# Kernel optimization log

Hardware: AMD Instinct MI355X
Metric: run time of the kernel (lower is better)

Reference implementation:

```python
import jax, jax.numpy as jnp
import numpy as np

DIM = 768
HEADS = 12
HEAD_DIM = DIM // HEADS
HIDDEN = 4 * DIM
SCALE = HEAD_DIM ** -0.5
LN_EPS = 1e-5


def _fit_poly_gelu():
    # replicate PolyGELU.__init__: quadratic least-squares fit to exact GELU on [-3,3]
    x = np.linspace(-3.0, 3.0, 10000).astype(np.float32)
    y = np.asarray(jax.nn.gelu(jnp.asarray(x), approximate=False))
    X = np.stack([x ** 2, x, np.ones_like(x)], axis=1)
    c, *_ = np.linalg.lstsq(X, y, rcond=None)
    return c.astype(np.float32)  # [a, b, c]


def setup_inputs() -> dict:
    key = jax.random.key(0)
    ks = jax.random.split(key, 8)
    g = _fit_poly_gelu()
    w = lambda k, shp: (jax.random.normal(k, shp, dtype=jnp.float32) * 0.02)
    return {
        "x": jax.random.normal(ks[0], (4, 2048, DIM), dtype=jnp.float32),
        "ln1_g": jnp.ones((DIM,), jnp.float32),
        "ln1_b": jnp.zeros((DIM,), jnp.float32),
        "ln2_g": jnp.ones((DIM,), jnp.float32),
        "ln2_b": jnp.zeros((DIM,), jnp.float32),
        "qkv_w": w(ks[1], (DIM, 3 * DIM)),   # stored [in, out]
        "qkv_b": jnp.zeros((3 * DIM,), jnp.float32),
        "proj_w": w(ks[2], (DIM, DIM)),
        "proj_b": jnp.zeros((DIM,), jnp.float32),
        "fc1_w": w(ks[3], (DIM, HIDDEN)),
        "fc1_b": jnp.zeros((HIDDEN,), jnp.float32),
        "fc2_w": w(ks[4], (HIDDEN, DIM)),
        "fc2_b": jnp.zeros((DIM,), jnp.float32),
        "attn_a": jnp.float32(0.05),
        "attn_b": jnp.float32(0.5),
        "attn_c": jnp.float32(0.25),
        "gelu_a": jnp.float32(g[0]),
        "gelu_b": jnp.float32(g[1]),
        "gelu_c": jnp.float32(g[2]),
    }


def _layernorm(x, gamma, beta):
    mu = jnp.mean(x, axis=-1, keepdims=True)
    var = jnp.mean(jnp.square(x - mu), axis=-1, keepdims=True)
    return (x - mu) / jnp.sqrt(var + LN_EPS) * gamma + beta


def reference(x, ln1_g, ln1_b, ln2_g, ln2_b, qkv_w, qkv_b, proj_w, proj_b,
              fc1_w, fc1_b, fc2_w, fc2_b, attn_a, attn_b, attn_c,
              gelu_a, gelu_b, gelu_c):
    B, N, C = x.shape
    # --- attention branch ---
    h = _layernorm(x, ln1_g, ln1_b)
    qkv = (h @ qkv_w + qkv_b).reshape(B, N, 3, HEADS, HEAD_DIM)
    q, k, v = (qkv[:, :, i].transpose(0, 2, 1, 3) for i in range(3))  # [B,H,N,D]
    attn = jnp.einsum("bhnd,bhmd->bhnm", q, k) * SCALE
    # poly_normed: quadratic activation, clamp, row-normalize
    attn = attn_a * attn * attn + attn_b * attn + attn_c
    attn = jnp.maximum(attn, 1e-6)
    attn = attn / (jnp.sum(attn, axis=-1, keepdims=True) + 1e-8)
    out = jnp.einsum("bhnm,bhmd->bhnd", attn, v).transpose(0, 2, 1, 3).reshape(B, N, C)
    x = x + (out @ proj_w + proj_b)
    # --- MLP branch with PolyGELU ---
    h = _layernorm(x, ln2_g, ln2_b)
    u = h @ fc1_w + fc1_b
    u = gelu_a * u * u + gelu_b * u + gelu_c
    x = x + (u @ fc2_w + fc2_b)
    return x
```

## Files before the change

### kernel.cpp

```cpp
#include <hip/hip_runtime.h>

typedef __bf16 bf16x8 __attribute__((ext_vector_type(8)));
typedef __bf16 bf16x4 __attribute__((ext_vector_type(4)));
typedef float f32x4 __attribute__((ext_vector_type(4)));
typedef unsigned int u32x4v __attribute__((ext_vector_type(4)));

#define LN_EPS 1e-5f

__device__ __forceinline__ void gl2lds16(const void* g, void* l) {
  __builtin_amdgcn_global_load_lds(
      (const __attribute__((address_space(1))) unsigned int*)g,
      (__attribute__((address_space(3))) unsigned int*)l, 16, 0, 0);
}

template <int KEEP>
__device__ __forceinline__ void pipe_barrier() {
  if constexpr (KEEP == 0)
    __asm__ __volatile__("s_waitcnt vmcnt(0) lgkmcnt(0)\n\ts_barrier" ::: "memory");
  else if constexpr (KEEP == 3)
    __asm__ __volatile__("s_waitcnt vmcnt(3) lgkmcnt(0)\n\ts_barrier" ::: "memory");
  else if constexpr (KEEP == 4)
    __asm__ __volatile__("s_waitcnt vmcnt(4) lgkmcnt(0)\n\ts_barrier" ::: "memory");
}

__device__ __forceinline__ unsigned cvt_pk_bf16(float lo, float hi) {
  unsigned r;
  asm("v_cvt_pk_bf16_f32 %0, %1, %2" : "=v"(r) : "v"(lo), "v"(hi));
  return r;
}
__device__ __forceinline__ void plane32_swap(unsigned& a, unsigned& b) {
  asm("v_permlane32_swap_b32 %0, %1" : "+v"(a), "+v"(b));
}
__device__ __forceinline__ void plane16_swap(unsigned& a, unsigned& b) {
  asm("v_permlane16_swap_b32 %0, %1" : "+v"(a), "+v"(b));
}

__global__ __launch_bounds__(256) void transpose_k(const float* __restrict__ in,
                                                   __bf16* __restrict__ out,
                                                   int R, int C) {
  __shared__ __bf16 t[32][33];
  int tx = threadIdx.x & 31, ty = threadIdx.x >> 5;
  int c = blockIdx.x * 32 + tx;
  for (int j = 0; j < 4; j++) {
    int r = blockIdx.y * 32 + ty + j * 8;
    t[ty + j * 8][tx] = (__bf16)in[(size_t)r * C + c];
  }
  __syncthreads();
  int r2 = blockIdx.y * 32 + tx;
  for (int j = 0; j < 4; j++) {
    int c2 = blockIdx.x * 32 + ty + j * 8;
    out[(size_t)c2 * R + r2] = t[tx][ty + j * 8];
  }
}

__global__ __launch_bounds__(256) void ln_kernel(const float* __restrict__ x,
                                                 const float* __restrict__ g,
                                                 const float* __restrict__ bta,
                                                 __bf16* __restrict__ out) {
  int row = blockIdx.x;
  size_t base = (size_t)row * 768;
  int t = threadIdx.x;
  float v[3];
  float s = 0.f, s2 = 0.f;
  for (int k = 0; k < 3; k++) {
    float f = x[base + t + k * 256];
    v[k] = f;
    s += f;
    s2 += f * f;
  }
  for (int m = 1; m < 64; m <<= 1) {
    s += __shfl_xor(s, m, 64);
    s2 += __shfl_xor(s2, m, 64);
  }
  __shared__ float sm[4][2];
  int wid = t >> 6, lane = t & 63;
  if (lane == 0) { sm[wid][0] = s; sm[wid][1] = s2; }
  __syncthreads();
  s = sm[0][0] + sm[1][0] + sm[2][0] + sm[3][0];
  s2 = sm[0][1] + sm[1][1] + sm[2][1] + sm[3][1];
  float mu = s * (1.f / 768.f);
  float var = s2 * (1.f / 768.f) - mu * mu;
  float rstd = rsqrtf(var + LN_EPS);
  for (int k = 0; k < 3; k++) {
    int c = t + k * 256;
    out[base + c] = (__bf16)((v[k] - mu) * rstd * g[c] + bta[c]);
  }
}

template <int MT, int NT, int EPI, bool SWAP, int WPB>
__global__ __launch_bounds__(256, WPB)
void gemm_pl(const __bf16* __restrict__ A, const __bf16* __restrict__ BT,
             const float* __restrict__ bias, const float* __restrict__ res,
             void* __restrict__ outv, __bf16* __restrict__ vtb,
             int M, int N, int K,
             const float* __restrict__ c0p, const float* __restrict__ c1p,
             const float* __restrict__ c2p) {
  __shared__ __bf16 As[3][MT][32];
  __shared__ __bf16 Bs[3][NT][32];
  constexpr int IW = MT / 32, JW = NT / 32;
  constexpr int S = MT / 64 + NT / 64;
  const int tid = threadIdx.x, lane = tid & 63, wid = tid >> 6;
  const int wr = wid >> 1, wc = wid & 1;
  const int mr = lane & 15, quad = lane >> 4;
  const int bx = SWAP ? blockIdx.y : blockIdx.x;
  const int by = SWAP ? blockIdx.x : blockIdx.y;
  const int m0 = by * MT, n0 = bx * NT;
  const int swzsrc = (((lane & 3) ^ ((lane >> 2) & 3)) * 8);
  const int srow = lane >> 2;
  const int ck = ((quad ^ (mr & 3)) * 8);

  f32x4 acc[IW][JW] = {};

  auto stage = [&](int k0, int buf) {
    for (int g = 0; g < MT / 64; g++) {
      int r0 = wid * (MT / 4) + g * 16 + srow;
      gl2lds16(&A[(size_t)(m0 + r0) * K + k0 + swzsrc], &As[buf][r0][(lane & 3) * 8]);
    }
    for (int g = 0; g < NT / 64; g++) {
      int r0 = wid * (NT / 4) + g * 16 + srow;
      gl2lds16(&BT[(size_t)(n0 + r0) * K + k0 + swzsrc], &Bs[buf][r0][(lane & 3) * 8]);
    }
  };

  const int T = K / 32;
  stage(0, 0);
  stage(32, 1);
  for (int it = 0; it < T; it++) {
    if (it < T - 1) pipe_barrier<S>(); else pipe_barrier<0>();
    if (it + 2 < T) stage((it + 2) * 32, (it + 2) % 3);
    const int pb = it % 3;
    bf16x8 af[IW], bfr[JW];
    for (int i = 0; i < IW; i++) af[i] = *(bf16x8*)&As[pb][wr * (MT / 2) + i * 16 + mr][ck];
    for (int j = 0; j < JW; j++) bfr[j] = *(bf16x8*)&Bs[pb][wc * (NT / 2) + j * 16 + mr][ck];
    for (int i = 0; i < IW; i++)
      for (int j = 0; j < JW; j++)
        acc[i][j] = __builtin_amdgcn_mfma_f32_16x16x32_bf16(af[i], bfr[j], acc[i][j], 0, 0, 0);
  }

  float ga = 0.f, gb = 0.f, gc = 0.f;
  if (EPI == 1) { ga = *c0p; gb = *c1p; gc = *c2p; }

  for (int i = 0; i < IW; i++) {
    for (int j = 0; j < JW; j++) {
      int col = n0 + wc * (NT / 2) + j * 16 + mr;
      float bv = bias[col];
      int row0 = m0 + wr * (MT / 2) + i * 16 + quad * 4;
      if (EPI == 3 && col >= 1536) {
        int hh = (col >> 6) - 24, dd = col & 63;
        bf16x4 pk;
        for (int r = 0; r < 4; r++) pk[r] = (__bf16)(acc[i][j][r] + bv);
        *(bf16x4*)&vtb[(((size_t)(row0 >> 11) * 12 + hh) * 64 + dd) * 2048 +
                       (row0 & 2047)] = pk;
      } else {
        for (int r = 0; r < 4; r++) {
          size_t idx = (size_t)(row0 + r) * N + col;
          float c = acc[i][j][r] + bv;
          if (EPI == 1) {
            float u = (ga * c + gb) * c + gc;
            ((__bf16*)outv)[idx] = (__bf16)u;
          } else if (EPI == 2) {
            ((float*)outv)[idx] = c + res[idx];
          } else {
            ((__bf16*)outv)[idx] = (__bf16)c;
          }
        }
      }
    }
  }
}

__global__ __launch_bounds__(256, 3) void attn_poly(const __bf16* __restrict__ qkv,
                                                    const __bf16* __restrict__ vt,
                                                    __bf16* __restrict__ outp,
                                                    const float* __restrict__ ap,
                                                    const float* __restrict__ bp,
                                                    const float* __restrict__ cp) {
  __shared__ __bf16 Kb[2][64][64];
  __shared__ __bf16 Vb[2][64][64];

  const int tid = threadIdx.x, lane = tid & 63, wid = tid >> 6;
  const int mr = lane & 15, quad = lane >> 4;
  const int bh = blockIdx.x;
  const int h = bh % 12, b = bh / 12;
  const int q0 = blockIdx.y * 128;
  const size_t baseQ = ((size_t)b * 2048) * 2304 + h * 64;

  const int swzsrc = (((lane & 7) ^ ((lane >> 3) & 7)) * 8);
  const int srow8 = lane >> 3;
  const int colS0 = ((quad ^ (mr & 7)) * 8);
  const int colS1 = (((4 + quad) ^ (mr & 7)) * 8);

  bf16x8 qf[2][2];
  for (int i = 0; i < 2; i++)
    for (int s = 0; s < 2; s++)
      qf[i][s] = *(const bf16x8*)&qkv[baseQ + (size_t)(q0 + wid * 32 + i * 16 + mr) * 2304 +
                                      s * 32 + quad * 8];

  const float a2 = (*ap) * 0.015625f, b2 = (*bp) * 0.125f, cc = *cp;
  f32x4 o_acc[2][4] = {};
  float l_acc[2] = {0.f, 0.f};

  auto stage = [&](int kt, int pb) {
    for (int g = 0; g < 2; g++) {
      int r0 = wid * 16 + g * 8 + srow8;
      gl2lds16(&qkv[baseQ + (size_t)(kt * 64 + r0) * 2304 + 768 + swzsrc],
               &Kb[pb][r0][(lane & 7) * 8]);
      gl2lds16(&vt[((size_t)bh * 64 + r0) * 2048 + kt * 64 + swzsrc],
               &Vb[pb][r0][(lane & 7) * 8]);
    }
  };

  stage(0, 0);
  int pb = 0;
  for (int kt = 0; kt < 32; kt++) {
    __syncthreads();
    if (kt < 31) stage(kt + 1, pb ^ 1);

    f32x4 sacc[2][4] = {};
    for (int j = 0; j < 4; j++) {
      for (int s = 0; s < 2; s++) {
        bf16x8 kf = *(bf16x8*)&Kb[pb][j * 16 + mr][s ? colS1 : colS0];
        for (int i = 0; i < 2; i++)
          sacc[i][j] = __builtin_amdgcn_mfma_f32_16x16x32_bf16(kf, qf[i][s], sacc[i][j], 0, 0, 0);
      }
    }

    bf16x8 pf[2][2];
    for (int i = 0; i < 2; i++) {
      unsigned w0[4], w1[4];
      f32x4 racc = {0.f, 0.f, 0.f, 0.f};
      for (int j = 0; j < 4; j++) {
        f32x4 S = sacc[i][j];
        f32x4 p = (a2 * S + b2) * S + cc;
        p[0] = fmaxf(p[0], 1e-6f); p[1] = fmaxf(p[1], 1e-6f);
        p[2] = fmaxf(p[2], 1e-6f); p[3] = fmaxf(p[3], 1e-6f);
        racc += p;
        w0[j] = cvt_pk_bf16(p[0], p[1]);
        w1[j] = cvt_pk_bf16(p[2], p[3]);
      }
      float rsum = racc[0] + racc[1] + racc[2] + racc[3];
      rsum += __shfl_xor(rsum, 16, 64);
      rsum += __shfl_xor(rsum, 32, 64);
      l_acc[i] += rsum;
      for (int s = 0; s < 2; s++) {
        unsigned a0 = w0[2 * s], b0 = w0[2 * s + 1];
        unsigned a1 = w1[2 * s], b1 = w1[2 * s + 1];
        plane32_swap(a0, b0); plane16_swap(a0, b0);
        plane32_swap(a1, b1); plane16_swap(a1, b1);
        u32x4v t = {a0, a1, b0, b1};
        pf[i][s] = __builtin_bit_cast(bf16x8, t);
      }
    }

    for (int s = 0; s < 2; s++) {
      for (int dt = 0; dt < 4; dt++) {
        bf16x8 vf = *(bf16x8*)&Vb[pb][dt * 16 + mr][s ? colS1 : colS0];
        for (int i = 0; i < 2; i++)
          o_acc[i][dt] = __builtin_amdgcn_mfma_f32_16x16x32_bf16(pf[i][s], vf, o_acc[i][dt], 0, 0, 0);
      }
    }
    pb ^= 1;
  }

  size_t baseO = ((size_t)b * 2048) * 768 + h * 64;
  for (int i = 0; i < 2; i++) {
    float inv[4];
    for (int r = 0; r < 4; r++)
      inv[r] = 1.0f / (__shfl(l_acc[i], quad * 4 + r, 64) + 1e-8f);
    for (int dt = 0; dt < 4; dt++) {
      int q = q0 + wid * 32 + i * 16 + quad * 4;
      for (int r = 0; r < 4; r++)
        outp[baseO + (size_t)(q + r) * 768 + dt * 16 + mr] =
            (__bf16)(o_acc[i][dt][r] * inv[r]);
    }
  }
}

extern "C" void kernel_launch(void* const* d_in, const int* in_sizes, int n_in,
                              void* d_out, int out_size, void* d_ws, size_t ws_size,
                              hipStream_t stream) {
  const float* x     = (const float*)d_in[0];
  const float* ln1g  = (const float*)d_in[1];
  const float* ln1b  = (const float*)d_in[2];
  const float* ln2g  = (const float*)d_in[3];
  const float* ln2b  = (const float*)d_in[4];
  const float* qkvw  = (const float*)d_in[5];
  const float* qkvb  = (const float*)d_in[6];
  const float* projw = (const float*)d_in[7];
  const float* projb = (const float*)d_in[8];
  const float* fc1w  = (const float*)d_in[9];
  const float* fc1b  = (const float*)d_in[10];
  const float* fc2w  = (const float*)d_in[11];
  const float* fc2b  = (const float*)d_in[12];
  const float* attna = (const float*)d_in[13];
  const float* attnb = (const float*)d_in[14];
  const float* attnc = (const float*)d_in[15];
  const float* gelua = (const float*)d_in[16];
  const float* gelub = (const float*)d_in[17];
  const float* geluc = (const float*)d_in[18];

  char* ws = (char*)d_ws;
  __bf16* wT_qkv  = (__bf16*)(ws);
  __bf16* wT_proj = (__bf16*)(ws + 3538944);
  __bf16* wT_fc1  = (__bf16*)(ws + 4718592);
  __bf16* wT_fc2  = (__bf16*)(ws + 9437184);
  __bf16* h       = (__bf16*)(ws + 14155776);
  float*  x1      = (float*)(ws + 26738688);
  __bf16* qkvbuf  = (__bf16*)(ws + 51904512);
  __bf16* u       = (__bf16*)(ws + 51904512);
  __bf16* vtbuf   = (__bf16*)(ws + 89653248);
  float*  outp    = (float*)d_out;

  transpose_k<<<dim3(2304 / 32, 768 / 32), 256, 0, stream>>>(qkvw, wT_qkv, 768, 2304);
  transpose_k<<<dim3(768 / 32, 768 / 32), 256, 0, stream>>>(projw, wT_proj, 768, 768);
  transpose_k<<<dim3(3072 / 32, 768 / 32), 256, 0, stream>>>(fc1w, wT_fc1, 768, 3072);
  transpose_k<<<dim3(768 / 32, 3072 / 32), 256, 0, stream>>>(fc2w, wT_fc2, 3072, 768);

  ln_kernel<<<8192, 256, 0, stream>>>(x, ln1g, ln1b, h);
  gemm_pl<128, 128, 3, false, 3><<<dim3(18, 64), 256, 0, stream>>>(
      h, wT_qkv, qkvb, nullptr, qkvbuf, vtbuf, 8192, 2304, 768, nullptr, nullptr, nullptr);
  attn_poly<<<dim3(48, 16), 256, 0, stream>>>(qkvbuf, vtbuf, h, attna, attnb, attnc);
  gemm_pl<64, 128, 2, true, 4><<<dim3(128, 6), 256, 0, stream>>>(
      h, wT_proj, projb, x, x1, nullptr, 8192, 768, 768, nullptr, nullptr, nullptr);
  ln_kernel<<<8192, 256, 0, stream>>>(x1, ln2g, ln2b, h);
  gemm_pl<128, 128, 1, false, 3><<<dim3(24, 64), 256, 0, stream>>>(
      h, wT_fc1, fc1b, nullptr, u, nullptr, 8192, 3072, 768, gelua, gelub, geluc);
  gemm_pl<64, 128, 2, true, 4><<<dim3(128, 6), 256, 0, stream>>>(
      u, wT_fc2, fc2b, x1, outp, nullptr, 8192, 768, 3072, nullptr, nullptr, nullptr);
}
```

Baseline: 399.0 us.

## Hoist staging addresses, defer row-sum reduction, add MFMA priority hints

In both the GEMM and attention kernels, global and LDS staging pointers are now computed once and advanced incrementally, so each stage no longer recomputes the address arithmetic. The attention kernel keeps its row sums as per-lane vector accumulators and does the cross-lane shuffle reduction once after the loop, which removes shuffles from every key tile. MFMA blocks are wrapped with s_setprio so the matrix-math waves are favoured over the others. The first score MFMA also takes a zero operand directly, so sacc no longer needs zero-initialising. Together these cut scalar and VALU overhead inside the hot loops, but the extra pointer live ranges may raise register pressure.

```diff
diff --git a/kernel.cpp b/kernel.cpp
--- a/kernel.cpp
+++ b/kernel.cpp
@@ -111,15 +111,17 @@
 
   f32x4 acc[IW][JW] = {};
 
+  const size_t gK = (size_t)16 * K;
+  const __bf16* aS = A + (size_t)(m0 + wid * (MT / 4) + srow) * K + swzsrc;
+  const __bf16* bS = BT + (size_t)(n0 + wid * (NT / 4) + srow) * K + swzsrc;
+  __bf16* dA0 = &As[0][wid * (MT / 4) + srow][(lane & 3) * 8];
+  __bf16* dB0 = &Bs[0][wid * (NT / 4) + srow][(lane & 3) * 8];
+
   auto stage = [&](int k0, int buf) {
-    for (int g = 0; g < MT / 64; g++) {
-      int r0 = wid * (MT / 4) + g * 16 + srow;
-      gl2lds16(&A[(size_t)(m0 + r0) * K + k0 + swzsrc], &As[buf][r0][(lane & 3) * 8]);
-    }
-    for (int g = 0; g < NT / 64; g++) {
-      int r0 = wid * (NT / 4) + g * 16 + srow;
-      gl2lds16(&BT[(size_t)(n0 + r0) * K + k0 + swzsrc], &Bs[buf][r0][(lane & 3) * 8]);
-    }
+    __bf16* da = dA0 + buf * (MT * 32);
+    __bf16* db = dB0 + buf * (NT * 32);
+    for (int g = 0; g < MT / 64; g++) gl2lds16(aS + k0 + g * gK, da + g * 512);
+    for (int g = 0; g < NT / 64; g++) gl2lds16(bS + k0 + g * gK, db + g * 512);
   };
 
   const int T = K / 32;
@@ -132,9 +134,11 @@
     bf16x8 af[IW], bfr[JW];
     for (int i = 0; i < IW; i++) af[i] = *(bf16x8*)&As[pb][wr * (MT / 2) + i * 16 + mr][ck];
     for (int j = 0; j < JW; j++) bfr[j] = *(bf16x8*)&Bs[pb][wc * (NT / 2) + j * 16 + mr][ck];
+    __builtin_amdgcn_s_setprio(1);
     for (int i = 0; i < IW; i++)
       for (int j = 0; j < JW; j++)
         acc[i][j] = __builtin_amdgcn_mfma_f32_16x16x32_bf16(af[i], bfr[j], acc[i][j], 0, 0, 0);
+    __builtin_amdgcn_s_setprio(0);
   }
 
   float ga = 0.f, gb = 0.f, gc = 0.f;
@@ -198,50 +202,57 @@
 
   const float a2 = (*ap) * 0.015625f, b2 = (*bp) * 0.125f, cc = *cp;
   f32x4 o_acc[2][4] = {};
-  float l_acc[2] = {0.f, 0.f};
-
-  auto stage = [&](int kt, int pb) {
-    for (int g = 0; g < 2; g++) {
-      int r0 = wid * 16 + g * 8 + srow8;
-      gl2lds16(&qkv[baseQ + (size_t)(kt * 64 + r0) * 2304 + 768 + swzsrc],
-               &Kb[pb][r0][(lane & 7) * 8]);
-      gl2lds16(&vt[((size_t)bh * 64 + r0) * 2048 + kt * 64 + swzsrc],
-               &Vb[pb][r0][(lane & 7) * 8]);
-    }
+  f32x4 lv[2] = {};
+  const f32x4 z4 = {0.f, 0.f, 0.f, 0.f};
+
+  const __bf16* kp = qkv + baseQ + 768 + (size_t)(wid * 16 + srow8) * 2304 + swzsrc;
+  const __bf16* vp = vt + ((size_t)bh * 64 + wid * 16 + srow8) * 2048 + swzsrc;
+  __bf16* kd0 = &Kb[0][wid * 16 + srow8][(lane & 7) * 8];
+  __bf16* vd0 = &Vb[0][wid * 16 + srow8][(lane & 7) * 8];
+
+  auto stage = [&](const __bf16* kpp, const __bf16* vpp, int pbuf) {
+    __bf16* kd = kd0 + pbuf * 4096;
+    __bf16* vd = vd0 + pbuf * 4096;
+    gl2lds16(kpp, kd);
+    gl2lds16(kpp + 8 * 2304, kd + 512);
+    gl2lds16(vpp, vd);
+    gl2lds16(vpp + 8 * 2048, vd + 512);
   };
 
-  stage(0, 0);
+  stage(kp, vp, 0);
+  const __bf16* kpn = kp + 64 * 2304;
+  const __bf16* vpn = vp + 64;
   int pb = 0;
   for (int kt = 0; kt < 32; kt++) {
     __syncthreads();
-    if (kt < 31) stage(kt + 1, pb ^ 1);
-
-    f32x4 sacc[2][4] = {};
+    if (kt < 31) { stage(kpn, vpn, pb ^ 1); kpn += 64 * 2304; vpn += 64; }
+    const __bf16* kb = &Kb[pb][0][0];
+    const __bf16* vb = &Vb[pb][0][0];
+
+    f32x4 sacc[2][4];
+    __builtin_amdgcn_s_setprio(1);
     for (int j = 0; j < 4; j++) {
-      for (int s = 0; s < 2; s++) {
-        bf16x8 kf = *(bf16x8*)&Kb[pb][j * 16 + mr][s ? colS1 : colS0];
-        for (int i = 0; i < 2; i++)
-          sacc[i][j] = __builtin_amdgcn_mfma_f32_16x16x32_bf16(kf, qf[i][s], sacc[i][j], 0, 0, 0);
-      }
-    }
+      bf16x8 kf0 = *(bf16x8*)(kb + (j * 16 + mr) * 64 + colS0);
+      bf16x8 kf1 = *(bf16x8*)(kb + (j * 16 + mr) * 64 + colS1);
+      for (int i = 0; i < 2; i++) {
+        sacc[i][j] = __builtin_amdgcn_mfma_f32_16x16x32_bf16(kf0, qf[i][0], z4, 0, 0, 0);
+        sacc[i][j] = __builtin_amdgcn_mfma_f32_16x16x32_bf16(kf1, qf[i][1], sacc[i][j], 0, 0, 0);
+      }
+    }
+    __builtin_amdgcn_s_setprio(0);
 
     bf16x8 pf[2][2];
     for (int i = 0; i < 2; i++) {
       unsigned w0[4], w1[4];
-      f32x4 racc = {0.f, 0.f, 0.f, 0.f};
       for (int j = 0; j < 4; j++) {
         f32x4 S = sacc[i][j];
         f32x4 p = (a2 * S + b2) * S + cc;
         p[0] = fmaxf(p[0], 1e-6f); p[1] = fmaxf(p[1], 1e-6f);
         p[2] = fmaxf(p[2], 1e-6f); p[3] = fmaxf(p[3], 1e-6f);
-        racc += p;
+        lv[i] += p;
         w0[j] = cvt_pk_bf16(p[0], p[1]);
         w1[j] = cvt_pk_bf16(p[2], p[3]);
       }
-      float rsum = racc[0] + racc[1] + racc[2] + racc[3];
-      rsum += __shfl_xor(rsum, 16, 64);
-      rsum += __shfl_xor(rsum, 32, 64);
-      l_acc[i] += rsum;
       for (int s = 0; s < 2; s++) {
         unsigned a0 = w0[2 * s], b0 = w0[2 * s + 1];
         unsigned a1 = w1[2 * s], b1 = w1[2 * s + 1];
@@ -252,14 +263,24 @@
       }
     }
 
+    __builtin_amdgcn_s_setprio(1);
     for (int s = 0; s < 2; s++) {
       for (int dt = 0; dt < 4; dt++) {
-        bf16x8 vf = *(bf16x8*)&Vb[pb][dt * 16 + mr][s ? colS1 : colS0];
+        bf16x8 vf = *(bf16x8*)(vb + (dt * 16 + mr) * 64 + (s ? colS1 : colS0));
         for (int i = 0; i < 2; i++)
           o_acc[i][dt] = __builtin_amdgcn_mfma_f32_16x16x32_bf16(pf[i][s], vf, o_acc[i][dt], 0, 0, 0);
       }
     }
+    __builtin_amdgcn_s_setprio(0);
     pb ^= 1;
+  }
+
+  float l_acc[2];
+  for (int i = 0; i < 2; i++) {
+    float rsum = lv[i][0] + lv[i][1] + lv[i][2] + lv[i][3];
+    rsum += __shfl_xor(rsum, 16, 64);
+    rsum += __shfl_xor(rsum, 32, 64);
+    l_acc[i] = rsum;
   }
 
   size_t baseO = ((size_t)b * 2048) * 768 + h * 64;
```

Result: no change. 391.5 us (-1.9%).
